# Optimization experiments

Hardware: AMD Instinct MI355X
Metric: run time of the kernel (lower is better)

The kernel has to match this reference:

```python
import jax, jax.numpy as jnp
import numpy as np

EPS = 1e-10        # matches eps in calculate_jeffreys_similarity
NEG = -1e30        # finite 'masked out' logit (avoids NaN for absent classes)
NORM_EPS = 1e-12   # F.normalize clamp


def setup_inputs() -> dict:
    key = jax.random.key(0)
    k1, k2, k3 = jax.random.split(key, 3)
    B, D, H, W = 4, 256, 256, 256
    C, P = 16, 5
    feature_map = jax.random.normal(k1, (B, D, H, W), dtype=jnp.float32)
    prototypes = jax.random.normal(k2, (C * P, D), dtype=jnp.float32)
    gt_mask = jax.random.randint(k3, (B, H, W), 0, C, dtype=jnp.int32)
    return {
        "feature_map": feature_map,
        "prototypes": prototypes,
        "gt_mask": gt_mask,
        "num_prototypes_per_class": P,
    }


def _loss(feature_map, prototypes, gt_mask, P):
    B, D, H, W = feature_map.shape
    N = H * W
    C = prototypes.shape[0] // P

    # [B, N, D] L2-normalized pixel features (F.normalize, eps=1e-12)
    feats = feature_map.reshape(B, D, N).transpose(0, 2, 1)
    feats = feats / jnp.maximum(jnp.linalg.norm(feats, axis=-1, keepdims=True), NORM_EPS)

    # [C, P, D] L2-normalized prototypes
    protos = prototypes.reshape(C, P, D)
    protos = protos / jnp.maximum(jnp.linalg.norm(protos, axis=-1, keepdims=True), NORM_EPS)

    # per-class pixel membership mask [B, C, N]
    mask = gt_mask.reshape(B, 1, N) == jnp.arange(C, dtype=gt_mask.dtype)[None, :, None]
    present = jnp.any(mask, axis=-1)                        # [B, C]

    # cosine similarities: [B, C, P, N]
    sims = jnp.einsum('bnd,cpd->bcpn', feats, protos)

    m = mask[:, :, None, :]                                 # [B, C, 1, N]
    # first softmax over the pixels of the class (original: softmax(similarities, dim=0))
    s1 = jax.nn.softmax(jnp.where(m, sims, NEG), axis=-1)
    # second softmax applied inside calculate_jeffreys_similarity (over the same gathered pixels)
    s2 = jax.nn.softmax(jnp.where(m, s1, NEG), axis=-1)

    # V = distribution + eps; off-mask positions are exactly eps, and since
    # eps*(log eps - log eps)=0 they contribute nothing to the KL sums below,
    # so summing over all N reproduces the gathered-pixel sum exactly.
    V = jnp.where(m, s2, 0.0) + EPS                          # [B, C, P, N]
    logV = jnp.log(V)

    A = jnp.sum(V * logV, axis=-1)                           # [B, C, P]
    # Bmat[b,c,i,j] = sum_n logV[i] * V[j]
    Bmat = jnp.einsum('bcin,bcjn->bcij', logV, V)
    # KL(V_j || V_i) = A[j] - Bmat[i, j]
    M = A[:, :, None, :] - Bmat                              # [B, C, P, P]
    J = M + jnp.swapaxes(M, -1, -2)                          # Jeffreys divergence (symmetric)
    simmat = jnp.exp(-J)                                     # pairwise similarity

    P_ = simmat.shape[-1]
    triu = jnp.triu(jnp.ones((P_, P_), dtype=simmat.dtype), k=1)
    num_pairs = P_ * (P_ - 1) // 2
    class_sim = jnp.sum(simmat * triu, axis=(-1, -2)) / num_pairs   # [B, C]

    # mean over classes that actually appear in the image; empty image -> 0
    class_sim = jnp.where(present, class_sim, 0.0)
    cnt = jnp.sum(present, axis=-1).astype(class_sim.dtype)          # [B]
    batch_loss = jnp.where(cnt > 0, jnp.sum(class_sim, axis=-1) / jnp.maximum(cnt, 1.0), 0.0)
    return jnp.sum(batch_loss) / B


def reference(feature_map, prototypes, gt_mask, num_prototypes_per_class):
    return _loss(feature_map, prototypes, gt_mask, num_prototypes_per_class)
```

## Files before the change

### kernel.cpp

```cpp
#include <hip/hip_runtime.h>
#include <math.h>

#define BB 4
#define DD 256
#define NN 65536
#define CC 16
#define PP 5
#define CP 80
#define EPSV 1e-10f
#define PITCH 264

#define OFF_PLANE  20480
#define OFF_ACC    (OFF_PLANE + BB * PP * NN)
#define ACC_FLOATS (320 + 320 + 64 + BB * CC * 16)

__device__ __forceinline__ unsigned short f2bf(float f) {
    unsigned int u = __float_as_uint(f);
    u += 0x7fffu + ((u >> 16) & 1u);
    return (unsigned short)(u >> 16);
}

__global__ void k_norm(const float* __restrict__ protos,
                       float* __restrict__ protosN,
                       float* __restrict__ acc) {
    if (blockIdx.x == CP) {
        for (int i = threadIdx.x; i < ACC_FLOATS; i += 256) acc[i] = 0.f;
        return;
    }
    int r = blockIdx.x;
    int d = threadIdx.x;
    float v = protos[r * DD + d];
    __shared__ float red[256];
    red[d] = v * v;
    __syncthreads();
    for (int s = 128; s > 0; s >>= 1) {
        if (d < s) red[d] += red[d + s];
        __syncthreads();
    }
    float inv = 1.f / fmaxf(sqrtf(red[0]), 1e-12f);
    protosN[r * DD + d] = v * inv;
}

__device__ __forceinline__ void loadg(const float* __restrict__ fb, int g,
                                      float2 (&f)[8]) {
    const float* p = fb + (size_t)g * 8 * NN;
    #pragma unroll
    for (int k = 0; k < 8; ++k)
        f[k] = *reinterpret_cast<const float2*>(p + (size_t)k * NN);
}

__device__ __forceinline__ void comp(const char* lb0, const char* lb1,
                                     const float2 (&f)[8], int g,
                                     float (&d0)[PP], float (&d1)[PP],
                                     float& n0, float& n1) {
    uint4 q0[PP], q1[PP];
    #pragma unroll
    for (int p = 0; p < PP; ++p) {
        q0[p] = *reinterpret_cast<const uint4*>(lb0 + p * (PITCH * 2) + g * 16);
        q1[p] = *reinterpret_cast<const uint4*>(lb1 + p * (PITCH * 2) + g * 16);
    }
    #pragma unroll
    for (int k = 0; k < 8; ++k) {
        float fx = f[k].x, fy = f[k].y;
        n0 = fmaf(fx, fx, n0);
        n1 = fmaf(fy, fy, n1);
        #pragma unroll
        for (int p = 0; p < PP; ++p) {
            unsigned int w0 = (&q0[p].x)[k >> 1];
            unsigned int w1 = (&q1[p].x)[k >> 1];
            float a = __uint_as_float((k & 1) ? (w0 & 0xffff0000u) : (w0 << 16));
            float c = __uint_as_float((k & 1) ? (w1 & 0xffff0000u) : (w1 << 16));
            d0[p] = fmaf(fx, a, d0[p]);
            d1[p] = fmaf(fy, c, d1[p]);
        }
    }
}

__global__ __launch_bounds__(256) void k_sims(const float* __restrict__ fmap,
                                              const float* __restrict__ protosN,
                                              const int* __restrict__ gt,
                                              float* __restrict__ plane,
                                              float* __restrict__ denom1,
                                              float* __restrict__ cnt) {
    __shared__ __align__(16) unsigned short lp[CP * PITCH];
    __shared__ float bins[CP];
    __shared__ float binc[CC];
    const int tid = threadIdx.x;
    const int b   = blockIdx.x >> 7;
    const int n0  = ((blockIdx.x & 127) << 9) + (tid << 1);

    if (tid < CP) bins[tid] = 0.f;
    if (tid < CC) binc[tid] = 0.f;

    for (int idx = tid; idx < 5120; idx += 256) {
        int cp = idx >> 6, q = idx & 63;
        float4 v = *reinterpret_cast<const float4*>(&protosN[(cp << 8) + (q << 2)]);
        unsigned int u0 = (unsigned int)f2bf(v.x) | ((unsigned int)f2bf(v.y) << 16);
        unsigned int u1 = (unsigned int)f2bf(v.z) | ((unsigned int)f2bf(v.w) << 16);
        *reinterpret_cast<uint2*>(reinterpret_cast<char*>(lp) + cp * (PITCH * 2) + (q << 3))
            = make_uint2(u0, u1);
    }
    __syncthreads();

    const int2 cls = *reinterpret_cast<const int2*>(&gt[(size_t)b * NN + n0]);
    const char* lb0 = reinterpret_cast<const char*>(lp) + cls.x * (PP * PITCH * 2);
    const char* lb1 = reinterpret_cast<const char*>(lp) + cls.y * (PP * PITCH * 2);
    const float* fb = fmap + (size_t)b * DD * NN + n0;

    float dot0[PP] = {0.f, 0.f, 0.f, 0.f, 0.f};
    float dot1[PP] = {0.f, 0.f, 0.f, 0.f, 0.f};
    float nrm0 = 0.f, nrm1 = 0.f;
    float2 fA[8], fB[8];

    loadg(fb, 0, fA);
    #pragma unroll 1
    for (int g = 0; g < 32; g += 2) {
        loadg(fb, g + 1, fB);
        comp(lb0, lb1, fA, g, dot0, dot1, nrm0, nrm1);
        if (g < 30) loadg(fb, g + 2, fA);
        comp(lb0, lb1, fB, g + 1, dot0, dot1, nrm0, nrm1);
    }

    const float inv0 = 1.f / fmaxf(sqrtf(nrm0), 1e-12f);
    const float inv1 = 1.f / fmaxf(sqrtf(nrm1), 1e-12f);
    #pragma unroll
    for (int p = 0; p < PP; ++p) {
        float2 e;
        e.x = __expf(dot0[p] * inv0 - 1.f);
        e.y = __expf(dot1[p] * inv1 - 1.f);
        *reinterpret_cast<float2*>(&plane[(size_t)(b * PP + p) * NN + n0]) = e;
        atomicAdd(&bins[cls.x * PP + p], e.x);
        atomicAdd(&bins[cls.y * PP + p], e.y);
    }
    atomicAdd(&binc[cls.x], 1.f);
    atomicAdd(&binc[cls.y], 1.f);
    __syncthreads();
    if (tid < CP) atomicAdd(&denom1[b * CP + tid], bins[tid]);
    if (tid < CC) atomicAdd(&cnt[b * CC + tid], binc[tid]);
}

__global__ __launch_bounds__(256) void k_denom2(const int* __restrict__ gt,
                                                const float* __restrict__ plane,
                                                const float* __restrict__ denom1,
                                                float* __restrict__ denom2) {
    __shared__ float inv1s[CP];
    __shared__ float bins[4][CP];
    const int tid = threadIdx.x;
    const int w   = tid >> 6;
    const int b   = blockIdx.x >> 6;
    const int n0  = ((blockIdx.x & 63) << 10) + (tid << 2);
    if (tid < CP) inv1s[tid] = 1.f / denom1[b * CP + tid];
    for (int i = tid; i < 4 * CP; i += 256) (&bins[0][0])[i] = 0.f;
    __syncthreads();
    const int4 cls = *reinterpret_cast<const int4*>(&gt[(size_t)b * NN + n0]);
    #pragma unroll
    for (int p = 0; p < PP; ++p) {
        size_t idx = (size_t)(b * PP + p) * NN + n0;
        float4 e = *reinterpret_cast<const float4*>(&plane[idx]);
        atomicAdd(&bins[w][cls.x * PP + p], __expf(e.x * inv1s[cls.x * PP + p] - 1.f));
        atomicAdd(&bins[w][cls.y * PP + p], __expf(e.y * inv1s[cls.y * PP + p] - 1.f));
        atomicAdd(&bins[w][cls.z * PP + p], __expf(e.z * inv1s[cls.z * PP + p] - 1.f));
        atomicAdd(&bins[w][cls.w * PP + p], __expf(e.w * inv1s[cls.w * PP + p] - 1.f));
    }
    __syncthreads();
    if (tid < CP)
        atomicAdd(&denom2[b * CP + tid],
                  bins[0][tid] + bins[1][tid] + bins[2][tid] + bins[3][tid]);
}

__global__ __launch_bounds__(256) void k_bmat(const int* __restrict__ gt,
                                              const float* __restrict__ plane,
                                              const float* __restrict__ denom1,
                                              const float* __restrict__ denom2,
                                              float* __restrict__ Bbins) {
    __shared__ float inv1s[CP];
    __shared__ float inv2s[CP];
    __shared__ float sb[4][CC * 16];
    const int tid = threadIdx.x;
    const int w   = tid >> 6;
    const int b   = blockIdx.x >> 6;
    const int n0  = ((blockIdx.x & 63) << 10) + (tid << 2);
    if (tid < CP) {
        inv1s[tid] = 1.f / denom1[b * CP + tid];
        inv2s[tid] = 1.f / denom2[b * CP + tid];
    }
    for (int i = tid; i < 4 * CC * 16; i += 256) (&sb[0][0])[i] = 0.f;
    __syncthreads();
    const int4 cls = *reinterpret_cast<const int4*>(&gt[(size_t)b * NN + n0]);
    const int c4[4] = {cls.x, cls.y, cls.z, cls.w};
    float V[4][PP], L[4][PP];
    #pragma unroll
    for (int p = 0; p < PP; ++p) {
        size_t idx = (size_t)(b * PP + p) * NN + n0;
        float4 e = *reinterpret_cast<const float4*>(&plane[idx]);
        V[0][p] = fmaf(__expf(e.x * inv1s[cls.x * PP + p] - 1.f), inv2s[cls.x * PP + p], EPSV);
        V[1][p] = fmaf(__expf(e.y * inv1s[cls.y * PP + p] - 1.f), inv2s[cls.y * PP + p], EPSV);
        V[2][p] = fmaf(__expf(e.z * inv1s[cls.z * PP + p] - 1.f), inv2s[cls.z * PP + p], EPSV);
        V[3][p] = fmaf(__expf(e.w * inv1s[cls.w * PP + p] - 1.f), inv2s[cls.w * PP + p], EPSV);
    }
    #pragma unroll
    for (int q = 0; q < 4; ++q)
        #pragma unroll
        for (int p = 0; p < PP; ++p) L[q][p] = __logf(V[q][p]);
    #pragma unroll
    for (int q = 0; q < 4; ++q) {
        float* base = &sb[w][c4[q] * 16];
        #pragma unroll
        for (int i = 0; i < PP; ++i) atomicAdd(&base[i], L[q][i] * V[q][i]);
        int slot = 5;
        #pragma unroll
        for (int i = 0; i < PP; ++i)
            #pragma unroll
            for (int j = i + 1; j < PP; ++j) {
                atomicAdd(&base[slot], fmaf(L[q][i], V[q][j], L[q][j] * V[q][i]));
                ++slot;
            }
    }
    __syncthreads();
    for (int i = tid; i < CC * 16; i += 256)
        atomicAdd(&Bbins[b * CC * 16 + i], sb[0][i] + sb[1][i] + sb[2][i] + sb[3][i]);
}

__global__ void k_final(const float* __restrict__ Bbins,
                        const float* __restrict__ cnt,
                        float* __restrict__ out) {
    __shared__ float cs[BB * CC];
    __shared__ float pr[BB * CC];
    const int t = threadIdx.x;
    if (t < BB * CC) {
        const float* bb = &Bbins[t * 16];
        float s = 0.f;
        int slot = 5;
        #pragma unroll
        for (int i = 0; i < PP; ++i)
            for (int j = i + 1; j < PP; ++j) {
                float J = bb[i] + bb[j] - bb[slot];
                ++slot;
                s += __expf(-J);
            }
        bool present = cnt[t] > 0.f;
        cs[t] = present ? s * 0.1f : 0.f;
        pr[t] = present ? 1.f : 0.f;
    }
    __syncthreads();
    if (t == 0) {
        float total = 0.f;
        for (int b = 0; b < BB; ++b) {
            float sc = 0.f, np = 0.f;
            for (int c = 0; c < CC; ++c) { sc += cs[b * CC + c]; np += pr[b * CC + c]; }
            total += (np > 0.f) ? sc / np : 0.f;
        }
        out[0] = total / (float)BB;
    }
}

extern "C" void kernel_launch(void* const* d_in, const int* in_sizes, int n_in,
                              void* d_out, int out_size, void* d_ws, size_t ws_size,
                              hipStream_t stream) {
    const float* fmap   = (const float*)d_in[0];
    const float* protos = (const float*)d_in[1];
    const int*   gt     = (const int*)d_in[2];
    float* ws      = (float*)d_ws;
    float* protosN = ws;
    float* plane   = ws + OFF_PLANE;
    float* acc     = ws + OFF_ACC;
    float* denom1  = acc;
    float* denom2  = acc + 320;
    float* cnt     = acc + 640;
    float* Bbins   = acc + 704;
    float* out     = (float*)d_out;

    k_norm  <<<CP + 1, 256, 0, stream>>>(protos, protosN, acc);
    k_sims  <<<512, 256, 0, stream>>>(fmap, protosN, gt, plane, denom1, cnt);
    k_denom2<<<256, 256, 0, stream>>>(gt, plane, denom1, denom2);
    k_bmat  <<<256, 256, 0, stream>>>(gt, plane, denom1, denom2, Bbins);
    k_final <<<1, 64, 0, stream>>>(Bbins, cnt, out);
}
```

Before: 93.77 us.

## Stage feature loads through LDS with async global_load_lds double buffering

Replaces per-thread register prefetch of feature-map columns with asynchronous global-to-LDS loads into a per-wave double buffer, using explicit vmcnt waits. The prototype bf16 table is now loaded in two halves of the D dimension, which shrinks its LDS footprint and makes room for the staging buffers. The aim is deeper memory-latency hiding with fewer registers on a bandwidth-bound kernel. In exchange it adds LDS traffic, extra block-wide barriers and hand-written waitcnt assembly that must be correct.

```diff
diff --git a/kernel.cpp b/kernel.cpp
--- a/kernel.cpp
+++ b/kernel.cpp
@@ -8,16 +8,22 @@
 #define PP 5
 #define CP 80
 #define EPSV 1e-10f
-#define PITCH 264
+#define PBYTES 272
 
 #define OFF_PLANE  20480
 #define OFF_ACC    (OFF_PLANE + BB * PP * NN)
 #define ACC_FLOATS (320 + 320 + 64 + BB * CC * 16)
 
-__device__ __forceinline__ unsigned short f2bf(float f) {
+__device__ __forceinline__ unsigned int f2bf(float f) {
     unsigned int u = __float_as_uint(f);
     u += 0x7fffu + ((u >> 16) & 1u);
-    return (unsigned short)(u >> 16);
+    return u >> 16;
+}
+
+__device__ __forceinline__ void gload_lds16(const float* g, void* l) {
+    __builtin_amdgcn_global_load_lds(
+        (const __attribute__((address_space(1))) unsigned int*)g,
+        (__attribute__((address_space(3))) unsigned int*)l, 16, 0, 0);
 }
 
 __global__ void k_norm(const float* __restrict__ protos,
@@ -41,14 +47,6 @@
     protosN[r * DD + d] = v * inv;
 }
 
-__device__ __forceinline__ void loadg(const float* __restrict__ fb, int g,
-                                      float2 (&f)[8]) {
-    const float* p = fb + (size_t)g * 8 * NN;
-    #pragma unroll
-    for (int k = 0; k < 8; ++k)
-        f[k] = *reinterpret_cast<const float2*>(p + (size_t)k * NN);
-}
-
 __device__ __forceinline__ void comp(const char* lb0, const char* lb1,
                                      const float2 (&f)[8], int g,
                                      float (&d0)[PP], float (&d1)[PP],
@@ -56,8 +54,8 @@
     uint4 q0[PP], q1[PP];
     #pragma unroll
     for (int p = 0; p < PP; ++p) {
-        q0[p] = *reinterpret_cast<const uint4*>(lb0 + p * (PITCH * 2) + g * 16);
-        q1[p] = *reinterpret_cast<const uint4*>(lb1 + p * (PITCH * 2) + g * 16);
+        q0[p] = *reinterpret_cast<const uint4*>(lb0 + p * PBYTES + g * 16);
+        q1[p] = *reinterpret_cast<const uint4*>(lb1 + p * PBYTES + g * 16);
     }
     #pragma unroll
     for (int k = 0; k < 8; ++k) {
@@ -82,43 +80,78 @@
                                               float* __restrict__ plane,
                                               float* __restrict__ denom1,
                                               float* __restrict__ cnt) {
-    __shared__ __align__(16) unsigned short lp[CP * PITCH];
+    __shared__ __align__(16) unsigned short lpp[CP * (PBYTES / 2)];
+    __shared__ __align__(16) char fstage[4][2][4096];
     __shared__ float bins[CP];
     __shared__ float binc[CC];
-    const int tid = threadIdx.x;
-    const int b   = blockIdx.x >> 7;
-    const int n0  = ((blockIdx.x & 127) << 9) + (tid << 1);
+    const int tid  = threadIdx.x;
+    const int wave = tid >> 6;
+    const int lane = tid & 63;
+    const int b    = blockIdx.x >> 7;
+    const int N0   = (blockIdx.x & 127) << 9;
+    const int n0   = N0 + (tid << 1);
+    const int nw   = N0 + (wave << 7);
 
     if (tid < CP) bins[tid] = 0.f;
     if (tid < CC) binc[tid] = 0.f;
 
-    for (int idx = tid; idx < 5120; idx += 256) {
-        int cp = idx >> 6, q = idx & 63;
-        float4 v = *reinterpret_cast<const float4*>(&protosN[(cp << 8) + (q << 2)]);
-        unsigned int u0 = (unsigned int)f2bf(v.x) | ((unsigned int)f2bf(v.y) << 16);
-        unsigned int u1 = (unsigned int)f2bf(v.z) | ((unsigned int)f2bf(v.w) << 16);
-        *reinterpret_cast<uint2*>(reinterpret_cast<char*>(lp) + cp * (PITCH * 2) + (q << 3))
-            = make_uint2(u0, u1);
-    }
-    __syncthreads();
-
     const int2 cls = *reinterpret_cast<const int2*>(&gt[(size_t)b * NN + n0]);
-    const char* lb0 = reinterpret_cast<const char*>(lp) + cls.x * (PP * PITCH * 2);
-    const char* lb1 = reinterpret_cast<const char*>(lp) + cls.y * (PP * PITCH * 2);
-    const float* fb = fmap + (size_t)b * DD * NN + n0;
+    const float* fwb = fmap + (size_t)b * DD * NN + nw;
+    const int lrow = lane >> 5;
+    const int lcol = (lane & 31) << 2;
 
     float dot0[PP] = {0.f, 0.f, 0.f, 0.f, 0.f};
     float dot1[PP] = {0.f, 0.f, 0.f, 0.f, 0.f};
     float nrm0 = 0.f, nrm1 = 0.f;
-    float2 fA[8], fB[8];
-
-    loadg(fb, 0, fA);
+
     #pragma unroll 1
-    for (int g = 0; g < 32; g += 2) {
-        loadg(fb, g + 1, fB);
-        comp(lb0, lb1, fA, g, dot0, dot1, nrm0, nrm1);
-        if (g < 30) loadg(fb, g + 2, fA);
-        comp(lb0, lb1, fB, g + 1, dot0, dot1, nrm0, nrm1);
+    for (int ch = 0; ch < 2; ++ch) {
+        __syncthreads();
+        #pragma unroll 1
+        for (int it = 0; it < 10; ++it) {
+            int idx = tid + (it << 8);
+            int cp = idx >> 5, q = idx & 31;
+            float4 v = *reinterpret_cast<const float4*>(
+                &protosN[(cp << 8) + (ch << 7) + (q << 2)]);
+            unsigned int u0 = f2bf(v.x) | (f2bf(v.y) << 16);
+            unsigned int u1 = f2bf(v.z) | (f2bf(v.w) << 16);
+            *reinterpret_cast<uint2*>(reinterpret_cast<char*>(lpp) + cp * PBYTES + (q << 3))
+                = make_uint2(u0, u1);
+        }
+        __syncthreads();
+
+        const char* lb0 = reinterpret_cast<const char*>(lpp) + cls.x * (PP * PBYTES);
+        const char* lb1 = reinterpret_cast<const char*>(lpp) + cls.y * (PP * PBYTES);
+        const int dbase = ch << 7;
+
+        #pragma unroll
+        for (int i = 0; i < 4; ++i)
+            gload_lds16(fwb + (size_t)(dbase + 2 * i + lrow) * NN + lcol,
+                        &fstage[wave][0][i * 1024]);
+        #pragma unroll
+        for (int i = 0; i < 4; ++i)
+            gload_lds16(fwb + (size_t)(dbase + 8 + 2 * i + lrow) * NN + lcol,
+                        &fstage[wave][1][i * 1024]);
+
+        #pragma unroll 1
+        for (int g = 0; g < 16; ++g) {
+            if (g < 15) asm volatile("s_waitcnt vmcnt(4)" ::: "memory");
+            else        asm volatile("s_waitcnt vmcnt(0)" ::: "memory");
+            const char* fs = &fstage[wave][g & 1][0];
+            float2 f[8];
+            #pragma unroll
+            for (int i = 0; i < 8; ++i)
+                f[i] = *reinterpret_cast<const float2*>(fs + i * 512 + (lane << 3));
+            asm volatile("s_waitcnt lgkmcnt(0)" ::: "memory");
+            if (g < 14) {
+                const int d0 = dbase + (g + 2) * 8;
+                #pragma unroll
+                for (int i = 0; i < 4; ++i)
+                    gload_lds16(fwb + (size_t)(d0 + 2 * i + lrow) * NN + lcol,
+                                &fstage[wave][g & 1][i * 1024]);
+            }
+            comp(lb0, lb1, f, g, dot0, dot1, nrm0, nrm1);
+        }
     }
 
     const float inv0 = 1.f / fmaxf(sqrtf(nrm0), 1e-12f);
```

After: 98.11 us. +4.6%, slower.

## Fuse denom2, bmat and final into one cooperative kernel with grid syncs

Applied to the files above, without the earlier changes.

Merges the second-softmax denominator pass, the pairwise KL accumulation pass and the final reduction into a single cooperative kernel separated by grid-wide barriers. The exp values from the first pass stay in registers, so the plane is read once instead of twice and two kernel launches are removed. The shared bins are padded to a stride of 17 to cut bank conflicts. In exchange it relies on cooperative launch with 256 co-resident blocks and pays two grid.sync costs.

```diff
diff --git a/kernel.cpp b/kernel.cpp
--- a/kernel.cpp
+++ b/kernel.cpp
@@ -1,5 +1,8 @@
 #include <hip/hip_runtime.h>
+#include <hip/hip_cooperative_groups.h>
 #include <math.h>
+
+namespace cg = cooperative_groups;
 
 #define BB 4
 #define DD 256
@@ -139,72 +142,65 @@
     if (tid < CC) atomicAdd(&cnt[b * CC + tid], binc[tid]);
 }
 
-__global__ __launch_bounds__(256) void k_denom2(const int* __restrict__ gt,
-                                                const float* __restrict__ plane,
-                                                const float* __restrict__ denom1,
-                                                float* __restrict__ denom2) {
+__global__ __launch_bounds__(256) void k_tail(const int* __restrict__ gt,
+                                              const float* __restrict__ plane,
+                                              float* __restrict__ acc,
+                                              float* __restrict__ out) {
+    cg::grid_group grid = cg::this_grid();
+    float* denom1 = acc;
+    float* denom2 = acc + 320;
+    float* cnt    = acc + 640;
+    float* Bbins  = acc + 704;
+
     __shared__ float inv1s[CP];
-    __shared__ float bins[4][CP];
+    __shared__ float wbins[4][CP];
+    __shared__ float inv2s[CP];
+    __shared__ float sb[4][CC * 17];
+
     const int tid = threadIdx.x;
     const int w   = tid >> 6;
     const int b   = blockIdx.x >> 6;
     const int n0  = ((blockIdx.x & 63) << 10) + (tid << 2);
+
     if (tid < CP) inv1s[tid] = 1.f / denom1[b * CP + tid];
-    for (int i = tid; i < 4 * CP; i += 256) (&bins[0][0])[i] = 0.f;
+    for (int i = tid; i < 4 * CP; i += 256) (&wbins[0][0])[i] = 0.f;
     __syncthreads();
     const int4 cls = *reinterpret_cast<const int4*>(&gt[(size_t)b * NN + n0]);
+    const int c4[4] = {cls.x, cls.y, cls.z, cls.w};
+    float u[4][PP];
     #pragma unroll
     for (int p = 0; p < PP; ++p) {
         size_t idx = (size_t)(b * PP + p) * NN + n0;
         float4 e = *reinterpret_cast<const float4*>(&plane[idx]);
-        atomicAdd(&bins[w][cls.x * PP + p], __expf(e.x * inv1s[cls.x * PP + p] - 1.f));
-        atomicAdd(&bins[w][cls.y * PP + p], __expf(e.y * inv1s[cls.y * PP + p] - 1.f));
-        atomicAdd(&bins[w][cls.z * PP + p], __expf(e.z * inv1s[cls.z * PP + p] - 1.f));
-        atomicAdd(&bins[w][cls.w * PP + p], __expf(e.w * inv1s[cls.w * PP + p] - 1.f));
+        u[0][p] = __expf(e.x * inv1s[cls.x * PP + p] - 1.f);
+        u[1][p] = __expf(e.y * inv1s[cls.y * PP + p] - 1.f);
+        u[2][p] = __expf(e.z * inv1s[cls.z * PP + p] - 1.f);
+        u[3][p] = __expf(e.w * inv1s[cls.w * PP + p] - 1.f);
+        atomicAdd(&wbins[w][cls.x * PP + p], u[0][p]);
+        atomicAdd(&wbins[w][cls.y * PP + p], u[1][p]);
+        atomicAdd(&wbins[w][cls.z * PP + p], u[2][p]);
+        atomicAdd(&wbins[w][cls.w * PP + p], u[3][p]);
     }
     __syncthreads();
     if (tid < CP)
         atomicAdd(&denom2[b * CP + tid],
-                  bins[0][tid] + bins[1][tid] + bins[2][tid] + bins[3][tid]);
-}
-
-__global__ __launch_bounds__(256) void k_bmat(const int* __restrict__ gt,
-                                              const float* __restrict__ plane,
-                                              const float* __restrict__ denom1,
-                                              const float* __restrict__ denom2,
-                                              float* __restrict__ Bbins) {
-    __shared__ float inv1s[CP];
-    __shared__ float inv2s[CP];
-    __shared__ float sb[4][CC * 16];
-    const int tid = threadIdx.x;
-    const int w   = tid >> 6;
-    const int b   = blockIdx.x >> 6;
-    const int n0  = ((blockIdx.x & 63) << 10) + (tid << 2);
-    if (tid < CP) {
-        inv1s[tid] = 1.f / denom1[b * CP + tid];
-        inv2s[tid] = 1.f / denom2[b * CP + tid];
-    }
-    for (int i = tid; i < 4 * CC * 16; i += 256) (&sb[0][0])[i] = 0.f;
-    __syncthreads();
-    const int4 cls = *reinterpret_cast<const int4*>(&gt[(size_t)b * NN + n0]);
-    const int c4[4] = {cls.x, cls.y, cls.z, cls.w};
+                  wbins[0][tid] + wbins[1][tid] + wbins[2][tid] + wbins[3][tid]);
+    grid.sync();
+
+    if (tid < CP) inv2s[tid] = 1.f / denom2[b * CP + tid];
+    for (int i = tid; i < 4 * CC * 17; i += 256) (&sb[0][0])[i] = 0.f;
+    __syncthreads();
     float V[4][PP], L[4][PP];
     #pragma unroll
-    for (int p = 0; p < PP; ++p) {
-        size_t idx = (size_t)(b * PP + p) * NN + n0;
-        float4 e = *reinterpret_cast<const float4*>(&plane[idx]);
-        V[0][p] = fmaf(__expf(e.x * inv1s[cls.x * PP + p] - 1.f), inv2s[cls.x * PP + p], EPSV);
-        V[1][p] = fmaf(__expf(e.y * inv1s[cls.y * PP + p] - 1.f), inv2s[cls.y * PP + p], EPSV);
-        V[2][p] = fmaf(__expf(e.z * inv1s[cls.z * PP + p] - 1.f), inv2s[cls.z * PP + p], EPSV);
-        V[3][p] = fmaf(__expf(e.w * inv1s[cls.w * PP + p] - 1.f), inv2s[cls.w * PP + p], EPSV);
-    }
-    #pragma unroll
     for (int q = 0; q < 4; ++q)
         #pragma unroll
-        for (int p = 0; p < PP; ++p) L[q][p] = __logf(V[q][p]);
+        for (int p = 0; p < PP; ++p) {
+            V[q][p] = fmaf(u[q][p], inv2s[c4[q] * PP + p], EPSV);
+            L[q][p] = __logf(V[q][p]);
+        }
     #pragma unroll
     for (int q = 0; q < 4; ++q) {
-        float* base = &sb[w][c4[q] * 16];
+        float* base = &sb[w][c4[q] * 17];
         #pragma unroll
         for (int i = 0; i < PP; ++i) atomicAdd(&base[i], L[q][i] * V[q][i]);
         int slot = 5;
@@ -217,40 +213,42 @@
             }
     }
     __syncthreads();
-    for (int i = tid; i < CC * 16; i += 256)
-        atomicAdd(&Bbins[b * CC * 16 + i], sb[0][i] + sb[1][i] + sb[2][i] + sb[3][i]);
-}
-
-__global__ void k_final(const float* __restrict__ Bbins,
-                        const float* __restrict__ cnt,
-                        float* __restrict__ out) {
-    __shared__ float cs[BB * CC];
-    __shared__ float pr[BB * CC];
-    const int t = threadIdx.x;
-    if (t < BB * CC) {
-        const float* bb = &Bbins[t * 16];
-        float s = 0.f;
-        int slot = 5;
-        #pragma unroll
-        for (int i = 0; i < PP; ++i)
-            for (int j = i + 1; j < PP; ++j) {
-                float J = bb[i] + bb[j] - bb[slot];
-                ++slot;
-                s += __expf(-J);
+    {
+        int c = tid >> 4, s = tid & 15;
+        float t = sb[0][c * 17 + s] + sb[1][c * 17 + s]
+                + sb[2][c * 17 + s] + sb[3][c * 17 + s];
+        atomicAdd(&Bbins[b * 256 + (c << 4) + s], t);
+    }
+    grid.sync();
+
+    if (blockIdx.x == 0) {
+        __shared__ float cs[BB * CC];
+        __shared__ float pr[BB * CC];
+        if (tid < BB * CC) {
+            const float* bb = &Bbins[tid * 16];
+            float s = 0.f;
+            int slot = 5;
+            #pragma unroll
+            for (int i = 0; i < PP; ++i)
+                for (int j = i + 1; j < PP; ++j) {
+                    float J = bb[i] + bb[j] - bb[slot];
+                    ++slot;
+                    s += __expf(-J);
+                }
+            bool present = cnt[tid] > 0.f;
+            cs[tid] = present ? s * 0.1f : 0.f;
+            pr[tid] = present ? 1.f : 0.f;
+        }
+        __syncthreads();
+        if (tid == 0) {
+            float total = 0.f;
+            for (int bb2 = 0; bb2 < BB; ++bb2) {
+                float sc = 0.f, np = 0.f;
+                for (int c = 0; c < CC; ++c) { sc += cs[bb2 * CC + c]; np += pr[bb2 * CC + c]; }
+                total += (np > 0.f) ? sc / np : 0.f;
             }
-        bool present = cnt[t] > 0.f;
-        cs[t] = present ? s * 0.1f : 0.f;
-        pr[t] = present ? 1.f : 0.f;
-    }
-    __syncthreads();
-    if (t == 0) {
-        float total = 0.f;
-        for (int b = 0; b < BB; ++b) {
-            float sc = 0.f, np = 0.f;
-            for (int c = 0; c < CC; ++c) { sc += cs[b * CC + c]; np += pr[b * CC + c]; }
-            total += (np > 0.f) ? sc / np : 0.f;
-        }
-        out[0] = total / (float)BB;
+            out[0] = total / (float)BB;
+        }
     }
 }
 
@@ -264,15 +262,14 @@
     float* protosN = ws;
     float* plane   = ws + OFF_PLANE;
     float* acc     = ws + OFF_ACC;
-    float* denom1  = acc;
-    float* denom2  = acc + 320;
-    float* cnt     = acc + 640;
-    float* Bbins   = acc + 704;
     float* out     = (float*)d_out;
 
-    k_norm  <<<CP + 1, 256, 0, stream>>>(protos, protosN, acc);
-    k_sims  <<<512, 256, 0, stream>>>(fmap, protosN, gt, plane, denom1, cnt);
-    k_denom2<<<256, 256, 0, stream>>>(gt, plane, denom1, denom2);
-    k_bmat  <<<256, 256, 0, stream>>>(gt, plane, denom1, denom2, Bbins);
-    k_final <<<1, 64, 0, stream>>>(Bbins, cnt, out);
-}
+    k_norm<<<CP + 1, 256, 0, stream>>>(protos, protosN, acc);
+    k_sims<<<512, 256, 0, stream>>>(fmap, protosN, gt, plane, acc, acc + 640);
+
+    const int* gt_c = gt;
+    const float* plane_c = plane;
+    void* args[4] = {(void*)&gt_c, (void*)&plane_c, (void*)&acc, (void*)&out};
+    hipLaunchCooperativeKernel(reinterpret_cast<void*>(k_tail),
+                               dim3(256), dim3(256), args, 0, stream);
+}
```

Result: slower. 139.2 us (+48.5%).
